# Kernel optimization log

Measured on AMD Instinct MI355X. Metric: run time of the kernel, lower is better.

Reference implementation:

```python
import jax, jax.numpy as jnp
import numpy as np

D_HID = 512
N_HEADS = 16
D_HEAD = D_HID // N_HEADS  # 32
D_FFN = 2048
B, N = 4, 1024
FACTOR = 0.5 / np.sqrt(D_HEAD)
EPS = 1e-5


def layer_norm(x, g, b):
    m = x.mean(-1, keepdims=True)
    v = ((x - m) ** 2).mean(-1, keepdims=True)
    return (x - m) / jnp.sqrt(v + EPS) * g + b


def setup_inputs() -> dict:
    key = jax.random.key(0)
    ks = jax.random.split(key, 24)
    s = 0.02
    p = lambda k, shape: jax.random.normal(k, shape, jnp.float32) * s
    inp = {
        'H': jax.random.normal(ks[0], (B, N, D_HID), jnp.float32),
        'V': jax.random.normal(ks[1], (B, N, 3, D_HID), jnp.float32),
        'D_batch': jax.random.normal(ks[2], (B, N, N), jnp.float32),
        'rbf_bias': jax.random.normal(ks[3], (B, 1, N, N), jnp.float32),
        'H_mask': jax.random.randint(ks[4], (B, N), 0, 2, jnp.int32),
        # attention sublayer params
        'g1': jnp.ones((D_HID,), jnp.float32), 'beta1': jnp.zeros((D_HID,), jnp.float32),
        'Wq': p(ks[5], (D_HID, 4 * D_HID)), 'bq': p(ks[6], (4 * D_HID,)),
        'Wk': p(ks[7], (D_HID, 4 * D_HID)), 'bk': p(ks[8], (4 * D_HID,)),
        'Wv': p(ks[9], (D_HID, D_HID)), 'bv': p(ks[10], (D_HID,)),
        'Wvv': p(ks[11], (D_HID, D_HID)),
        'Wo': p(ks[12], (D_HID, D_HID)), 'bo': p(ks[13], (D_HID,)),
        'Wvo': p(ks[14], (D_HID, D_HID)),
        # GVP FFN sublayer params
        'g2': jnp.ones((D_HID,), jnp.float32), 'beta2': jnp.zeros((D_HID,), jnp.float32),
        'Wlv': p(ks[15], (D_HID, 2 * D_HID)),
        'W1': p(ks[16], (2 * D_HID, D_FFN)), 'b1f': p(ks[17], (D_FFN,)),
        'W2': p(ks[18], (D_FFN, 2 * D_HID)), 'b2f': p(ks[19], (2 * D_HID,)),
    }
    return inp


def ept_forward(H, V, D_batch, rbf_bias, H_mask, g1, beta1, Wq, bq, Wk, bk, Wv, bv,
                Wvv, Wo, bo, Wvo, g2, beta2, Wlv, W1, b1f, W2, b2f):
    b, n, d = H.shape
    # ---- attention sublayer (pre-LN on H only, residual on H and V) ----
    Hn = layer_norm(H, g1, beta1)
    Hq = (Hn @ Wq + bq).reshape(b, n, N_HEADS, 4 * D_HEAD)
    Hk = (Hn @ Wk + bk).reshape(b, n, N_HEADS, 4 * D_HEAD)
    Hv = (Hn @ Wv + bv).reshape(b, n, N_HEADS, D_HEAD)
    # vector values: [b,n,3,d] -> [b,n,heads,3*dh]
    Vv = (V @ Wvv).reshape(b, n, 3, N_HEADS, D_HEAD).transpose(0, 1, 3, 2, 4)
    Vv = Vv.reshape(b, n, N_HEADS, 3 * D_HEAD)
    V_attn = jnp.concatenate([Hv, Vv], axis=-1)  # [b,n,h,4*dh]
    bias = rbf_bias + D_batch[:, None]  # [b,1,n,n]
    keep = (H_mask != 0)[:, None, None, :]  # mask keys
    bias = jnp.where(keep, bias, -jnp.inf)
    logits = jnp.einsum('bnhd,bmhd->bhnm', Hq, Hk) * FACTOR + bias
    attn = jax.nn.softmax(logits, axis=-1)
    res = jnp.einsum('bhnm,bmhd->bnhd', attn, V_attn)  # [b,n,h,4*dh]
    H_res = res[..., :D_HEAD].reshape(b, n, d)
    V_res = res[..., D_HEAD:].reshape(b, n, N_HEADS, 3, D_HEAD)
    V_res = V_res.transpose(0, 1, 3, 2, 4).reshape(b, n, 3, d)
    H = H + H_res @ Wo + bo
    V = V + V_res @ Wvo
    # ---- GVP FFN sublayer (pre-LN on H only, residual) ----
    Hn2 = layer_norm(H, g2, beta2)
    Vp = V @ Wlv  # [b,n,3,2d]
    V1, V2 = Vp[..., :d], Vp[..., d:]
    scaler = jnp.concatenate([Hn2, jnp.sqrt((V1 ** 2).sum(axis=-2))], axis=-1)
    h = jax.nn.silu(scaler @ W1 + b1f) @ W2 + b2f  # [b,n,2d]
    H = H + h[..., :d]
    V = V + h[..., None, d:] * V2
    return H, V


def reference(H, V, D_batch, rbf_bias, H_mask, g1, beta1, Wq, bq, Wk, bk, Wv, bv,
              Wvv, Wo, bo, Wvo, g2, beta2, Wlv, W1, b1f, W2, b2f):
    return ept_forward(H, V, D_batch, rbf_bias, H_mask, g1, beta1, Wq, bq, Wk, bk,
                       Wv, bv, Wvv, Wo, bo, Wvo, g2, beta2, Wlv, W1, b1f, W2, b2f)
```

## Files before the change

### kernel.cpp

```cpp
#include <hip/hip_runtime.h>
#include <math.h>

#define NBATCH 4
#define NSEQ   1024
#define DHID   512
#define NHEADS 16
#define ROWS   (NBATCH*NSEQ)
#define VROWS  (ROWS*3)
#define ATT_FACTOR 0.08838834764831845f
#define LOG2E 1.4426950408889634f
#define F2 (ATT_FACTOR*LOG2E)
#define SM_SHIFT (16.0f*LOG2E)

typedef __attribute__((ext_vector_type(8))) short short8;
typedef __attribute__((ext_vector_type(4))) float floatx4;

__device__ __forceinline__ ushort f2bf(float x) {
  union { float f; unsigned u; } v; v.f = x;
  unsigned r = v.u + 0x7fff + ((v.u >> 16) & 1);
  return (ushort)(r >> 16);
}
__device__ __forceinline__ float bf2f(ushort u) {
  union { unsigned u; float f; } v; v.u = ((unsigned)u) << 16; return v.f;
}

template<int OBF>
__global__ __launch_bounds__(256) void ln_kernel(
    const float* __restrict__ x, void* __restrict__ y, int ystride,
    const float* __restrict__ g, const float* __restrict__ beta)
{
  int row = blockIdx.x;
  int t = threadIdx.x;
  const float* xr = x + (size_t)row * DHID;
  float2 v = ((const float2*)xr)[t];
  float s  = v.x + v.y;
  float ss = v.x*v.x + v.y*v.y;
  #pragma unroll
  for (int off = 32; off > 0; off >>= 1) {
    s  += __shfl_down(s, off);
    ss += __shfl_down(ss, off);
  }
  __shared__ float red[8];
  int w = t >> 6;
  if ((t & 63) == 0) { red[w*2] = s; red[w*2+1] = ss; }
  __syncthreads();
  s  = red[0] + red[2] + red[4] + red[6];
  ss = red[1] + red[3] + red[5] + red[7];
  float mean = s * (1.0f/DHID);
  float var  = ss * (1.0f/DHID) - mean*mean;
  float rstd = rsqrtf(var + 1e-5f);
  float2 gg = ((const float2*)g)[t];
  float2 bb = ((const float2*)beta)[t];
  float2 o;
  o.x = (v.x - mean) * rstd * gg.x + bb.x;
  o.y = (v.y - mean) * rstd * gg.y + bb.y;
  if constexpr (OBF) {
    ushort2 u = { f2bf(o.x), f2bf(o.y) };
    *(ushort2*)&((ushort*)y)[(size_t)row * ystride + 2*t] = u;
  } else {
    *(float2*)&((float*)y)[(size_t)row * ystride + 2*t] = o;
  }
}

struct WJobs {
  const float* src[9];
  ushort*      dst[9];
  int K[9];
  int N[9];
  int blk0[10];
};

__global__ __launch_bounds__(256) void wtrans_all_kernel(WJobs J)
{
  __shared__ float Ts[64][65];
  int bid = blockIdx.x;
  int j = 0;
  #pragma unroll
  for (int i = 1; i < 9; i++) if (bid >= J.blk0[i]) j = i;
  const float* W = J.src[j];
  ushort* Wt = J.dst[j];
  int K = J.K[j], N = J.N[j];
  int local = bid - J.blk0[j];
  int nx = N >> 6;
  int bx = local - (local / nx) * nx;
  int by = local / nx;
  int k0 = by*64, n0 = bx*64;
  int t = threadIdx.x;
  #pragma unroll
  for (int p = 0; p < 4; p++) {
    int f = p*256 + t;
    int r = f >> 4, c = (f & 15)*4;
    float4 v = *(const float4*)&W[(size_t)(k0+r)*N + n0 + c];
    Ts[r][c] = v.x; Ts[r][c+1] = v.y; Ts[r][c+2] = v.z; Ts[r][c+3] = v.w;
  }
  __syncthreads();
  #pragma unroll
  for (int p = 0; p < 2; p++) {
    int gidx = p*256 + t;
    int nr = gidx >> 3, kc = (gidx & 7)*8;
    ushort u[8];
    #pragma unroll
    for (int x = 0; x < 8; x++) u[x] = f2bf(Ts[kc+x][nr]);
    ushort4 a = {u[0],u[1],u[2],u[3]}, b4 = {u[4],u[5],u[6],u[7]};
    *(ushort4*)&Wt[(size_t)(n0+nr)*K + k0 + kc]     = a;
    *(ushort4*)&Wt[(size_t)(n0+nr)*K + k0 + kc + 4] = b4;
  }
}

__global__ __launch_bounds__(256) void conv_bf16_kernel(
    const float* __restrict__ x, ushort* __restrict__ y)
{
  int i = blockIdx.x*256 + threadIdx.x;
  float4 v = ((const float4*)x)[i];
  ushort4 u = { f2bf(v.x), f2bf(v.y), f2bf(v.z), f2bf(v.w) };
  ((ushort4*)y)[i] = u;
}

template<int ACT, int HAS_BIAS, int HAS_RES, int OUT_BF16, int DUAL>
__global__ __launch_bounds__(256) void gemm_mfma_kernel(
    const ushort* __restrict__ A, const ushort* __restrict__ Bt,
    const float* __restrict__ bias, const float* __restrict__ resid,
    void* __restrict__ Cv, ushort* __restrict__ C2,
    int M, int N, int K)
{
  __shared__ ushort As[128*32];
  __shared__ ushort Bs[128*32];
  int t = threadIdx.x;
  int w = t >> 6, lane = t & 63;
  int q16 = lane & 15, quad = lane >> 4;
  int m0 = blockIdx.y * 128, n0 = blockIdx.x * 128;
  int wm = (w & 1) * 64, wn = (w >> 1) * 64;

  int r0 = t >> 2;
  int c0 = (t & 3) * 8;
  const ushort* Ag = A  + (size_t)(m0 + r0) * K + c0;
  const ushort* Bg = Bt + (size_t)(n0 + r0) * K + c0;

  floatx4 acc[4][4];
  #pragma unroll
  for (int i = 0; i < 4; i++)
    #pragma unroll
    for (int j = 0; j < 4; j++) acc[i][j] = (floatx4){0.f,0.f,0.f,0.f};

  for (int k0 = 0; k0 < K; k0 += 32) {
    float4 av0 = *(const float4*)(Ag + k0);
    float4 av1 = *(const float4*)(Ag + (size_t)64*K + k0);
    float4 bv0 = *(const float4*)(Bg + k0);
    float4 bv1 = *(const float4*)(Bg + (size_t)64*K + k0);
    __syncthreads();
    *(float4*)&As[r0*32 + c0]        = av0;
    *(float4*)&As[(r0 + 64)*32 + c0] = av1;
    *(float4*)&Bs[r0*32 + c0]        = bv0;
    *(float4*)&Bs[(r0 + 64)*32 + c0] = bv1;
    __syncthreads();
    short8 af[4], bf[4];
    #pragma unroll
    for (int i = 0; i < 4; i++) {
      af[i] = *(const short8*)&As[(wm + i*16 + q16)*32 + quad*8];
      bf[i] = *(const short8*)&Bs[(wn + i*16 + q16)*32 + quad*8];
    }
    #pragma unroll
    for (int i = 0; i < 4; i++)
      #pragma unroll
      for (int j = 0; j < 4; j++)
        acc[i][j] = __builtin_amdgcn_mfma_f32_16x16x32_bf16(af[i], bf[j], acc[i][j], 0, 0, 0);
  }

  float* Cf = (float*)Cv;
  ushort* Cu = (ushort*)Cv;
  float bj[4];
  #pragma unroll
  for (int j = 0; j < 4; j++)
    bj[j] = HAS_BIAS ? bias[n0 + wn + j*16 + q16] : 0.f;
  #pragma unroll
  for (int i = 0; i < 4; i++) {
    #pragma unroll
    for (int r = 0; r < 4; r++) {
      int row = m0 + wm + i*16 + quad*4 + r;
      size_t base = (size_t)row * N;
      #pragma unroll
      for (int j = 0; j < 4; j++) {
        int col = n0 + wn + j*16 + q16;
        float v = acc[i][j][r] + bj[j];
        if constexpr (ACT == 1) v = v / (1.f + __expf(-v));
        if constexpr (HAS_RES) v += resid[base + col];
        if constexpr (OUT_BF16) Cu[base + col] = f2bf(v);
        else                    Cf[base + col] = v;
        if constexpr (DUAL) C2[base + col] = f2bf(v);
      }
    }
  }
}

__global__ __launch_bounds__(256) void bias2_kernel(
    const float* __restrict__ Db, const float* __restrict__ Rb,
    const int* __restrict__ Mask, ushort* __restrict__ Bc2)
{
  int i2 = blockIdx.x*256 + threadIdx.x;
  int e = i2 * 2;
  int b = e >> 20;
  int m = e & 1023;
  float2 d = *(const float2*)&Db[e];
  float2 r = *(const float2*)&Rb[e];
  ushort2 o;
  o.x = Mask[b*NSEQ + m]     ? f2bf((d.x + r.x)*LOG2E) : f2bf(-1e30f);
  o.y = Mask[b*NSEQ + m + 1] ? f2bf((d.y + r.y)*LOG2E) : f2bf(-1e30f);
  *(ushort2*)&Bc2[e] = o;
}

__global__ __launch_bounds__(256) void vtrans_kernel(
    const float* __restrict__ Hv, const float* __restrict__ Vvr, ushort* __restrict__ Vt)
{
  __shared__ float Ts[64][33];
  int t = threadIdx.x;
  int bh = blockIdx.z;
  int b = bh >> 4, h = bh & 15;
  int dt = blockIdx.y;
  int nt = blockIdx.x;
  int d0 = dt*32, n0 = nt*64;
  #pragma unroll
  for (int i = 0; i < 2; i++) {
    int nl = (t >> 3) + i*32;
    int c4 = (t & 7)*4;
    const float* src;
    if (dt == 0) src = &Hv[(size_t)(b*NSEQ + n0 + nl)*512 + h*32 + c4];
    else { int c = dt - 1; src = &Vvr[((size_t)(b*NSEQ + n0 + nl)*3 + c)*512 + h*32 + c4]; }
    float4 v = *(const float4*)src;
    Ts[nl][c4] = v.x; Ts[nl][c4+1] = v.y; Ts[nl][c4+2] = v.z; Ts[nl][c4+3] = v.w;
  }
  __syncthreads();
  int dl = t >> 3;
  int n8 = (t & 7)*8;
  ushort u[8];
  #pragma unroll
  for (int k = 0; k < 8; k++) u[k] = f2bf(Ts[n8+k][dl]);
  size_t ob = ((size_t)bh*128 + d0 + dl)*NSEQ + n0 + n8;
  ushort4 u0 = {u[0],u[1],u[2],u[3]}, u1 = {u[4],u[5],u[6],u[7]};
  *(ushort4*)&Vt[ob]     = u0;
  *(ushort4*)&Vt[ob + 4] = u1;
}

__global__ __launch_bounds__(256) void attn_mfma_kernel(
    const ushort* __restrict__ Q, const ushort* __restrict__ K,
    const ushort* __restrict__ Vt, const ushort* __restrict__ Bc2,
    ushort* __restrict__ HRES, ushort* __restrict__ VRES)
{
  __shared__ union {
    ushort q[64][136];
    struct { ushort k[32][136]; ushort v[128][40]; } kv;
  } S;
  __shared__ ushort Ps[4][16][40];

  int t = threadIdx.x;
  int w = t >> 6, lane = t & 63;
  int q16 = lane & 15, quad = lane >> 4;
  int h = blockIdx.x, qt = blockIdx.y, b = blockIdx.z;
  int q0 = qt * 64;

  #pragma unroll
  for (int i = 0; i < 4; i++) {
    int f = t + i*256;
    int r = f >> 4, c8 = f & 15;
    *(float4*)&S.q[r][c8*8] =
        *(const float4*)&Q[(size_t)(b*NSEQ + q0 + r)*2048 + h*128 + c8*8];
  }
  __syncthreads();
  short8 qf[4];
  #pragma unroll
  for (int c = 0; c < 4; c++)
    qf[c] = *(const short8*)&S.q[w*16 + q16][c*32 + quad*8];

  floatx4 o[8];
  #pragma unroll
  for (int i = 0; i < 8; i++) o[i] = (floatx4){0.f,0.f,0.f,0.f};
  float l_i[4] = {0.f,0.f,0.f,0.f};
  const ushort* bias_base = Bc2 + (size_t)(b*NSEQ + q0 + w*16)*NSEQ;

  for (int m0 = 0; m0 < NSEQ; m0 += 32) {
    __syncthreads();
    #pragma unroll
    for (int i = 0; i < 2; i++) {
      int f = t + i*256;
      int r = f >> 4, c8 = f & 15;
      *(float4*)&S.kv.k[r][c8*8] =
          *(const float4*)&K[(size_t)(b*NSEQ + m0 + r)*2048 + h*128 + c8*8];
    }
    #pragma unroll
    for (int i = 0; i < 2; i++) {
      int f = t + i*256;
      int d = f >> 2, g = f & 3;
      *(float4*)&S.kv.v[d][g*8] =
          *(const float4*)&Vt[((size_t)(b*NHEADS + h)*128 + d)*NSEQ + m0 + g*8];
    }
    __syncthreads();

    floatx4 s0 = (floatx4){0.f,0.f,0.f,0.f};
    floatx4 s1 = (floatx4){0.f,0.f,0.f,0.f};
    #pragma unroll
    for (int c = 0; c < 4; c++) {
      short8 k0 = *(const short8*)&S.kv.k[q16][c*32 + quad*8];
      short8 k1 = *(const short8*)&S.kv.k[q16 + 16][c*32 + quad*8];
      s0 = __builtin_amdgcn_mfma_f32_16x16x32_bf16(qf[c], k0, s0, 0, 0, 0);
      s1 = __builtin_amdgcn_mfma_f32_16x16x32_bf16(qf[c], k1, s1, 0, 0, 0);
    }
    #pragma unroll
    for (int i = 0; i < 4; i++) {
      int row = quad*4 + i;
      const ushort* bp = bias_base + (size_t)row*NSEQ + m0 + q16;
      float v0 = s0[i]*F2 + bf2f(bp[0]);
      float v1 = s1[i]*F2 + bf2f(bp[16]);
      float p0 = exp2f(v0 - SM_SHIFT);
      float p1 = exp2f(v1 - SM_SHIFT);
      Ps[w][row][q16]      = f2bf(p0);
      Ps[w][row][16 + q16] = f2bf(p1);
      l_i[i] += p0 + p1;
    }
    short8 pf = *(const short8*)&Ps[w][q16][quad*8];
    #pragma unroll
    for (int tt = 0; tt < 8; tt++) {
      short8 vf = *(const short8*)&S.kv.v[tt*16 + q16][quad*8];
      o[tt] = __builtin_amdgcn_mfma_f32_16x16x32_bf16(pf, vf, o[tt], 0, 0, 0);
    }
  }
  #pragma unroll
  for (int i = 0; i < 4; i++) {
    float l = l_i[i];
    l += __shfl_xor(l, 1); l += __shfl_xor(l, 2);
    l += __shfl_xor(l, 4); l += __shfl_xor(l, 8);
    float inv = 1.0f / l;
    int grow = b*NSEQ + q0 + w*16 + quad*4 + i;
    #pragma unroll
    for (int tt = 0; tt < 2; tt++)
      HRES[(size_t)grow*512 + h*32 + tt*16 + q16] = f2bf(o[tt][i] * inv);
    #pragma unroll
    for (int tt = 2; tt < 8; tt++) {
      int c = (tt - 2) >> 1;
      int jj = ((tt - 2) & 1)*16 + q16;
      VRES[((size_t)grow*3 + c)*512 + h*32 + jj] = f2bf(o[tt][i] * inv);
    }
  }
}

__global__ __launch_bounds__(256) void vnorm_kernel(
    const float* __restrict__ VP, ushort* __restrict__ SC)
{
  int idx = blockIdx.x*256 + threadIdx.x;
  int row = idx >> 9;
  int d = idx & 511;
  const float* p = VP + (size_t)row*3072 + d;
  float a = p[0], b = p[1024], c = p[2048];
  SC[(size_t)row*1024 + 512 + d] = f2bf(sqrtf(a*a + b*b + c*c));
}

__global__ __launch_bounds__(256) void finale_kernel(
    const float* __restrict__ HH, const float* __restrict__ VP,
    float* __restrict__ Hout, float* __restrict__ Vout)
{
  int idx = blockIdx.x*256 + threadIdx.x;
  if (idx < ROWS*DHID) {
    int row = idx >> 9;
    int d = idx & 511;
    Hout[idx] += HH[(size_t)row*1024 + d];
  } else {
    int k = idx - ROWS*DHID;
    int r3 = k >> 9;
    int d = k & 511;
    int row = r3 / 3;
    Vout[k] += HH[(size_t)row*1024 + 512 + d] * VP[(size_t)r3*1024 + 512 + d];
  }
}

extern "C" void kernel_launch(void* const* d_in, const int* in_sizes, int n_in,
                              void* d_out, int out_size, void* d_ws, size_t ws_size,
                              hipStream_t stream)
{
  const float* H    = (const float*)d_in[0];
  const float* V    = (const float*)d_in[1];
  const float* Db   = (const float*)d_in[2];
  const float* Rb   = (const float*)d_in[3];
  const int*   Mask = (const int*)d_in[4];
  const float* g1   = (const float*)d_in[5];
  const float* be1  = (const float*)d_in[6];
  const float* Wq   = (const float*)d_in[7];
  const float* bq   = (const float*)d_in[8];
  const float* Wk   = (const float*)d_in[9];
  const float* bkk  = (const float*)d_in[10];
  const float* Wv   = (const float*)d_in[11];
  const float* bv   = (const float*)d_in[12];
  const float* Wvv  = (const float*)d_in[13];
  const float* Wo   = (const float*)d_in[14];
  const float* bo   = (const float*)d_in[15];
  const float* Wvo  = (const float*)d_in[16];
  const float* g2   = (const float*)d_in[17];
  const float* be2  = (const float*)d_in[18];
  const float* Wlv  = (const float*)d_in[19];
  const float* W1   = (const float*)d_in[20];
  const float* b1f  = (const float*)d_in[21];
  const float* W2   = (const float*)d_in[22];
  const float* b2f  = (const float*)d_in[23];

  float* Hout = (float*)d_out;
  float* Vout = Hout + (size_t)ROWS*DHID;

  char* w = (char*)d_ws;
  const size_t MB = 1024*1024;
  const size_t KB = 1024;
  ushort* WqT  = (ushort*)(w + 0);
  ushort* WkT  = (ushort*)(w + 2048*KB);
  ushort* WvT  = (ushort*)(w + 4096*KB);
  ushort* WvvT = (ushort*)(w + 4608*KB);
  ushort* WoT  = (ushort*)(w + 5120*KB);
  ushort* WvoT = (ushort*)(w + 5632*KB);
  ushort* WlvT = (ushort*)(w + 6144*KB);
  ushort* W1T  = (ushort*)(w + 7168*KB);
  ushort* W2T  = (ushort*)(w + 11264*KB);
  ushort* HNbf = (ushort*)(w + 16*MB);
  ushort* Qbf  = (ushort*)(w + 20*MB);
  ushort* Kbf  = (ushort*)(w + 36*MB);
  float*  HVt  = (float*)(w + 52*MB);
  float*  VVr  = (float*)(w + 60*MB);
  ushort* Vbf  = (ushort*)(w + 84*MB);
  ushort* Vtb  = (ushort*)(w + 96*MB);
  ushort* Bc2  = (ushort*)(w + 112*MB);
  ushort* HRESbf = (ushort*)(w + 120*MB);
  ushort* VRESbf = (ushort*)(w + 124*MB);
  ushort* Voutbf = (ushort*)(w + 52*MB);
  float*  VP     = (float*)(w + 64*MB);
  ushort* SCbf   = (ushort*)(w + 112*MB);
  ushort* S1bf   = (ushort*)(w + 120*MB);
  float*  HHb    = (float*)(w + 16*MB);

  dim3 blk(256);

  WJobs J;
  const float* ws_[9] = {Wq, Wk, Wv, Wvv, Wo, Wvo, Wlv, W1, W2};
  ushort* wd_[9] = {WqT, WkT, WvT, WvvT, WoT, WvoT, WlvT, W1T, W2T};
  int wk_[9] = {512, 512, 512, 512, 512, 512, 512, 1024, 2048};
  int wn_[9] = {2048, 2048, 512, 512, 512, 512, 1024, 2048, 1024};
  int off = 0;
  for (int i = 0; i < 9; i++) {
    J.src[i] = ws_[i]; J.dst[i] = wd_[i]; J.K[i] = wk_[i]; J.N[i] = wn_[i];
    J.blk0[i] = off;
    off += (wn_[i] >> 6) * (wk_[i] >> 6);
  }
  J.blk0[9] = off;
  wtrans_all_kernel<<<off, blk, 0, stream>>>(J);

  ln_kernel<1><<<ROWS, blk, 0, stream>>>(H, HNbf, DHID, g1, be1);
  conv_bf16_kernel<<<(VROWS*DHID/4)/256, blk, 0, stream>>>(V, Vbf);

  gemm_mfma_kernel<0,1,0,1,0><<<dim3(16, 32), blk, 0, stream>>>(HNbf, WqT, bq,  nullptr, Qbf, nullptr, 4096, 2048, 512);
  gemm_mfma_kernel<0,1,0,1,0><<<dim3(16, 32), blk, 0, stream>>>(HNbf, WkT, bkk, nullptr, Kbf, nullptr, 4096, 2048, 512);
  gemm_mfma_kernel<0,1,0,0,0><<<dim3( 4, 32), blk, 0, stream>>>(HNbf, WvT, bv,  nullptr, HVt, nullptr, 4096, 512, 512);
  gemm_mfma_kernel<0,0,0,0,0><<<dim3( 4, 96), blk, 0, stream>>>(Vbf, WvvT, nullptr, nullptr, VVr, nullptr, 12288, 512, 512);

  bias2_kernel<<<(NBATCH*NSEQ*NSEQ/2)/256, blk, 0, stream>>>(Db, Rb, Mask, Bc2);
  vtrans_kernel<<<dim3(16, 4, 64), blk, 0, stream>>>(HVt, VVr, Vtb);

  attn_mfma_kernel<<<dim3(16, 16, 4), blk, 0, stream>>>(Qbf, Kbf, Vtb, Bc2, HRESbf, VRESbf);

  gemm_mfma_kernel<0,1,1,0,0><<<dim3(4, 32), blk, 0, stream>>>(HRESbf, WoT,  bo, H, Hout, nullptr, 4096, 512, 512);
  gemm_mfma_kernel<0,0,1,0,1><<<dim3(4, 96), blk, 0, stream>>>(VRESbf, WvoT, nullptr, V, Vout, Voutbf, 12288, 512, 512);

  ln_kernel<1><<<ROWS, blk, 0, stream>>>(Hout, SCbf, 1024, g2, be2);
  gemm_mfma_kernel<0,0,0,0,0><<<dim3(8, 96), blk, 0, stream>>>(Voutbf, WlvT, nullptr, nullptr, VP, nullptr, 12288, 1024, 512);
  vnorm_kernel<<<(ROWS*DHID)/256, blk, 0, stream>>>(VP, SCbf);

  gemm_mfma_kernel<1,1,0,1,0><<<dim3(16, 32), blk, 0, stream>>>(SCbf, W1T, b1f, nullptr, S1bf, nullptr, 4096, 2048, 1024);
  gemm_mfma_kernel<0,1,0,0,0><<<dim3( 8, 32), blk, 0, stream>>>(S1bf, W2T, b2f, nullptr, HHb, nullptr, 4096, 1024, 2048);

  finale_kernel<<<((ROWS + VROWS)*DHID)/256, blk, 0, stream>>>(HHb, VP, Hout, Vout);
}
```

Measured before the change: 514.6 us.

## Double-buffer GEMM via direct global-to-LDS loads and fuse QKV projection

```diff
diff --git a/kernel.cpp b/kernel.cpp
--- a/kernel.cpp
+++ b/kernel.cpp
@@ -14,6 +14,11 @@
 
 typedef __attribute__((ext_vector_type(8))) short short8;
 typedef __attribute__((ext_vector_type(4))) float floatx4;
+
+#define AS1 __attribute__((address_space(1)))
+#define AS3 __attribute__((address_space(3)))
+#define GLOAD_LDS16(g, l) \
+  __builtin_amdgcn_global_load_lds((const AS1 void*)(g), (AS3 void*)(l), 16, 0, 0)
 
 __device__ __forceinline__ ushort f2bf(float x) {
   union { float f; unsigned u; } v; v.f = x;
@@ -116,6 +121,15 @@
   ((ushort4*)y)[i] = u;
 }
 
+__global__ __launch_bounds__(256) void biascat_kernel(
+    const float* __restrict__ bq, const float* __restrict__ bk,
+    const float* __restrict__ bv, float* __restrict__ o)
+{
+  int i = blockIdx.x*256 + threadIdx.x;
+  float v = (i < 2048) ? bq[i] : (i < 4096 ? bk[i-2048] : bv[i-4096]);
+  o[i] = v;
+}
+
 template<int ACT, int HAS_BIAS, int HAS_RES, int OUT_BF16, int DUAL>
 __global__ __launch_bounds__(256) void gemm_mfma_kernel(
     const ushort* __restrict__ A, const ushort* __restrict__ Bt,
@@ -123,8 +137,8 @@
     void* __restrict__ Cv, ushort* __restrict__ C2,
     int M, int N, int K)
 {
-  __shared__ ushort As[128*32];
-  __shared__ ushort Bs[128*32];
+  __shared__ ushort As[2][128*32];
+  __shared__ ushort Bs[2][128*32];
   int t = threadIdx.x;
   int w = t >> 6, lane = t & 63;
   int q16 = lane & 15, quad = lane >> 4;
@@ -135,6 +149,7 @@
   int c0 = (t & 3) * 8;
   const ushort* Ag = A  + (size_t)(m0 + r0) * K + c0;
   const ushort* Bg = Bt + (size_t)(n0 + r0) * K + c0;
+  int wb = w * 512;
 
   floatx4 acc[4][4];
   #pragma unroll
@@ -142,29 +157,35 @@
     #pragma unroll
     for (int j = 0; j < 4; j++) acc[i][j] = (floatx4){0.f,0.f,0.f,0.f};
 
-  for (int k0 = 0; k0 < K; k0 += 32) {
-    float4 av0 = *(const float4*)(Ag + k0);
-    float4 av1 = *(const float4*)(Ag + (size_t)64*K + k0);
-    float4 bv0 = *(const float4*)(Bg + k0);
-    float4 bv1 = *(const float4*)(Bg + (size_t)64*K + k0);
-    __syncthreads();
-    *(float4*)&As[r0*32 + c0]        = av0;
-    *(float4*)&As[(r0 + 64)*32 + c0] = av1;
-    *(float4*)&Bs[r0*32 + c0]        = bv0;
-    *(float4*)&Bs[(r0 + 64)*32 + c0] = bv1;
-    __syncthreads();
-    short8 af[4], bf[4];
+  #define STAGE(buf, kk) do { \
+    GLOAD_LDS16(Ag + (kk),                 &As[buf][wb]); \
+    GLOAD_LDS16(Ag + (size_t)64*K + (kk),  &As[buf][2048 + wb]); \
+    GLOAD_LDS16(Bg + (kk),                 &Bs[buf][wb]); \
+    GLOAD_LDS16(Bg + (size_t)64*K + (kk),  &Bs[buf][2048 + wb]); \
+  } while (0)
+
+  STAGE(0, 0);
+  __syncthreads();
+
+  int nt = K >> 5;
+  int cur = 0;
+  for (int kt = 0; kt < nt; kt++) {
+    if (kt + 1 < nt) STAGE(cur ^ 1, (kt + 1) * 32);
+    short8 af[4], bf4[4];
     #pragma unroll
     for (int i = 0; i < 4; i++) {
-      af[i] = *(const short8*)&As[(wm + i*16 + q16)*32 + quad*8];
-      bf[i] = *(const short8*)&Bs[(wn + i*16 + q16)*32 + quad*8];
+      af[i]  = *(const short8*)&As[cur][(wm + i*16 + q16)*32 + quad*8];
+      bf4[i] = *(const short8*)&Bs[cur][(wn + i*16 + q16)*32 + quad*8];
     }
     #pragma unroll
     for (int i = 0; i < 4; i++)
       #pragma unroll
       for (int j = 0; j < 4; j++)
-        acc[i][j] = __builtin_amdgcn_mfma_f32_16x16x32_bf16(af[i], bf[j], acc[i][j], 0, 0, 0);
-  }
+        acc[i][j] = __builtin_amdgcn_mfma_f32_16x16x32_bf16(af[i], bf4[j], acc[i][j], 0, 0, 0);
+    __syncthreads();
+    cur ^= 1;
+  }
+  #undef STAGE
 
   float* Cf = (float*)Cv;
   ushort* Cu = (ushort*)Cv;
@@ -209,7 +230,8 @@
 }
 
 __global__ __launch_bounds__(256) void vtrans_kernel(
-    const float* __restrict__ Hv, const float* __restrict__ Vvr, ushort* __restrict__ Vt)
+    const ushort* __restrict__ QKV, const ushort* __restrict__ VVr,
+    ushort* __restrict__ Vt)
 {
   __shared__ float Ts[64][33];
   int t = threadIdx.x;
@@ -222,11 +244,12 @@
   for (int i = 0; i < 2; i++) {
     int nl = (t >> 3) + i*32;
     int c4 = (t & 7)*4;
-    const float* src;
-    if (dt == 0) src = &Hv[(size_t)(b*NSEQ + n0 + nl)*512 + h*32 + c4];
-    else { int c = dt - 1; src = &Vvr[((size_t)(b*NSEQ + n0 + nl)*3 + c)*512 + h*32 + c4]; }
-    float4 v = *(const float4*)src;
-    Ts[nl][c4] = v.x; Ts[nl][c4+1] = v.y; Ts[nl][c4+2] = v.z; Ts[nl][c4+3] = v.w;
+    const ushort* src;
+    if (dt == 0) src = &QKV[(size_t)(b*NSEQ + n0 + nl)*4608 + 4096 + h*32 + c4];
+    else { int c = dt - 1; src = &VVr[((size_t)(b*NSEQ + n0 + nl)*3 + c)*512 + h*32 + c4]; }
+    ushort4 v = *(const ushort4*)src;
+    Ts[nl][c4] = bf2f(v.x); Ts[nl][c4+1] = bf2f(v.y);
+    Ts[nl][c4+2] = bf2f(v.z); Ts[nl][c4+3] = bf2f(v.w);
   }
   __syncthreads();
   int dl = t >> 3;
@@ -241,7 +264,7 @@
 }
 
 __global__ __launch_bounds__(256) void attn_mfma_kernel(
-    const ushort* __restrict__ Q, const ushort* __restrict__ K,
+    const ushort* __restrict__ QKV,
     const ushort* __restrict__ Vt, const ushort* __restrict__ Bc2,
     ushort* __restrict__ HRES, ushort* __restrict__ VRES)
 {
@@ -262,7 +285,7 @@
     int f = t + i*256;
     int r = f >> 4, c8 = f & 15;
     *(float4*)&S.q[r][c8*8] =
-        *(const float4*)&Q[(size_t)(b*NSEQ + q0 + r)*2048 + h*128 + c8*8];
+        *(const float4*)&QKV[(size_t)(b*NSEQ + q0 + r)*4608 + h*128 + c8*8];
   }
   __syncthreads();
   short8 qf[4];
@@ -283,7 +306,7 @@
       int f = t + i*256;
       int r = f >> 4, c8 = f & 15;
       *(float4*)&S.kv.k[r][c8*8] =
-          *(const float4*)&K[(size_t)(b*NSEQ + m0 + r)*2048 + h*128 + c8*8];
+          *(const float4*)&QKV[(size_t)(b*NSEQ + m0 + r)*4608 + 2048 + h*128 + c8*8];
     }
     #pragma unroll
     for (int i = 0; i < 2; i++) {
@@ -414,21 +437,20 @@
   ushort* WlvT = (ushort*)(w + 6144*KB);
   ushort* W1T  = (ushort*)(w + 7168*KB);
   ushort* W2T  = (ushort*)(w + 11264*KB);
-  ushort* HNbf = (ushort*)(w + 16*MB);
-  ushort* Qbf  = (ushort*)(w + 20*MB);
-  ushort* Kbf  = (ushort*)(w + 36*MB);
-  float*  HVt  = (float*)(w + 52*MB);
-  float*  VVr  = (float*)(w + 60*MB);
-  ushort* Vbf  = (ushort*)(w + 84*MB);
-  ushort* Vtb  = (ushort*)(w + 96*MB);
-  ushort* Bc2  = (ushort*)(w + 112*MB);
-  ushort* HRESbf = (ushort*)(w + 120*MB);
-  ushort* VRESbf = (ushort*)(w + 124*MB);
-  ushort* Voutbf = (ushort*)(w + 52*MB);
-  float*  VP     = (float*)(w + 64*MB);
-  ushort* SCbf   = (ushort*)(w + 112*MB);
-  ushort* S1bf   = (ushort*)(w + 120*MB);
-  float*  HHb    = (float*)(w + 16*MB);
+  float*  Bqkv = (float*)(w + 15360*KB);
+  ushort* HNbf  = (ushort*)(w + 16*MB);
+  ushort* QKVbf = (ushort*)(w + 20*MB);
+  ushort* VVrbf = (ushort*)(w + 56*MB);
+  ushort* Vbf   = (ushort*)(w + 68*MB);
+  ushort* Vtb   = (ushort*)(w + 80*MB);
+  ushort* Bc2   = (ushort*)(w + 96*MB);
+  ushort* HRESbf = (ushort*)(w + 104*MB);
+  ushort* VRESbf = (ushort*)(w + 108*MB);
+  ushort* Voutbf = (ushort*)(w + 20*MB);
+  float*  VP     = (float*)(w + 56*MB);
+  ushort* SCbf   = (ushort*)(w + 104*MB);
+  ushort* S1bf   = (ushort*)(w + 112*MB);
+  float*  HHb    = (float*)(w + 32*MB);
 
   dim3 blk(256);
 
@@ -448,16 +470,15 @@
 
   ln_kernel<1><<<ROWS, blk, 0, stream>>>(H, HNbf, DHID, g1, be1);
   conv_bf16_kernel<<<(VROWS*DHID/4)/256, blk, 0, stream>>>(V, Vbf);
-
-  gemm_mfma_kernel<0,1,0,1,0><<<dim3(16, 32), blk, 0, stream>>>(HNbf, WqT, bq,  nullptr, Qbf, nullptr, 4096, 2048, 512);
-  gemm_mfma_kernel<0,1,0,1,0><<<dim3(16, 32), blk, 0, stream>>>(HNbf, WkT, bkk, nullptr, Kbf, nullptr, 4096, 2048, 512);
-  gemm_mfma_kernel<0,1,0,0,0><<<dim3( 4, 32), blk, 0, stream>>>(HNbf, WvT, bv,  nullptr, HVt, nullptr, 4096, 512, 512);
-  gemm_mfma_kernel<0,0,0,0,0><<<dim3( 4, 96), blk, 0, stream>>>(Vbf, WvvT, nullptr, nullptr, VVr, nullptr, 12288, 512, 512);
+  biascat_kernel<<<18, blk, 0, stream>>>(bq, bkk, bv, Bqkv);
+
+  gemm_mfma_kernel<0,1,0,1,0><<<dim3(36, 32), blk, 0, stream>>>(HNbf, WqT, Bqkv, nullptr, QKVbf, nullptr, 4096, 4608, 512);
+  gemm_mfma_kernel<0,0,0,1,0><<<dim3( 4, 96), blk, 0, stream>>>(Vbf, WvvT, nullptr, nullptr, VVrbf, nullptr, 12288, 512, 512);
 
   bias2_kernel<<<(NBATCH*NSEQ*NSEQ/2)/256, blk, 0, stream>>>(Db, Rb, Mask, Bc2);
-  vtrans_kernel<<<dim3(16, 4, 64), blk, 0, stream>>>(HVt, VVr, Vtb);
-
-  attn_mfma_kernel<<<dim3(16, 16, 4), blk, 0, stream>>>(Qbf, Kbf, Vtb, Bc2, HRESbf, VRESbf);
+  vtrans_kernel<<<dim3(16, 4, 64), blk, 0, stream>>>(QKVbf, VVrbf, Vtb);
+
+  attn_mfma_kernel<<<dim3(16, 16, 4), blk, 0, stream>>>(QKVbf, Vtb, Bc2, HRESbf, VRESbf);
 
   gemm_mfma_kernel<0,1,1,0,0><<<dim3(4, 32), blk, 0, stream>>>(HRESbf, WoT,  bo, H, Hout, nullptr, 4096, 512, 512);
   gemm_mfma_kernel<0,0,1,0,1><<<dim3(4, 96), blk, 0, stream>>>(VRESbf, WvoT, nullptr, V, Vout, Voutbf, 12288, 512, 512);
```

Result: faster. 493.7 us (-4.1%).
